# Optimization experiments

Hardware: AMD Instinct MI355X
Metric: run time of the kernel (lower is better)

The kernel has to match this reference:

```python
import jax, jax.numpy as jnp
import numpy as np

EPS = 1e-6
NUM_HEADS = 16

def _phi(x):
    # elu kernel feature map: elu(x) + 1 (ensures positivity)
    return jax.nn.elu(x) + 1.0

def setup_inputs() -> dict:
    key = jax.random.key(0)
    ks = jax.random.split(key, 5)
    B, S, D = 2, 2048, 1024
    scale = 1.0 / np.sqrt(D)  # mimic xavier-ish magnitude
    return {
        "x": jax.random.normal(ks[0], (B, S, D), dtype=jnp.float32),
        "Wq": jax.random.normal(ks[1], (D, D), dtype=jnp.float32) * scale,
        "bq": jnp.zeros((D,), dtype=jnp.float32),
        "Wk": jax.random.normal(ks[2], (D, D), dtype=jnp.float32) * scale,
        "bk": jnp.zeros((D,), dtype=jnp.float32),
        "Wv": jax.random.normal(ks[3], (D, D), dtype=jnp.float32) * scale,
        "bv": jnp.zeros((D,), dtype=jnp.float32),
        "Wo": jax.random.normal(ks[4], (D, D), dtype=jnp.float32) * scale,
        "bo": jnp.zeros((D,), dtype=jnp.float32),
    }

def reference(x, Wq, bq, Wk, bk, Wv, bv, Wo, bo):
    B, S, D = x.shape
    H = NUM_HEADS
    hd = D // H
    # projections (torch Linear: x @ W.T + b)
    q = (x @ Wq.T + bq).reshape(B, S, H, hd).transpose(0, 2, 1, 3)  # [B,H,S,d]
    k = (x @ Wk.T + bk).reshape(B, S, H, hd).transpose(0, 2, 1, 3)
    v = (x @ Wv.T + bv).reshape(B, S, H, hd).transpose(0, 2, 1, 3)
    q = _phi(q)
    k = _phi(k)
    # prefix sums of outer products k_t v_t^T and of k_t (causal linear attention)
    kv_cum = jnp.cumsum(k[..., :, None] * v[..., None, :], axis=2)  # [B,H,S,d,d]
    k_cum = jnp.cumsum(k, axis=2)                                   # [B,H,S,d]
    num = jnp.einsum('bhsd,bhsde->bhse', q, kv_cum)                 # [B,H,S,d]
    den = jnp.einsum('bhsd,bhsd->bhs', q, k_cum)                    # [B,H,S]
    out = num / (den[..., None] + EPS)
    out = out.transpose(0, 2, 1, 3).reshape(B, S, D)
    return out @ Wo.T + bo
```

## Files before the change

### kernel.cpp

```cpp
#include <hip/hip_runtime.h>

typedef unsigned short u16;
typedef __attribute__((ext_vector_type(8))) short bf16x8;
typedef __attribute__((ext_vector_type(4))) float f32x4;

#define DEVI static __device__ __forceinline__

DEVI u16 f2bf(float f) {
  union { float f; unsigned int u; } a; a.f = f;
  unsigned int u = a.u;
  u += 0x7fffu + ((u >> 16) & 1u);
  return (u16)(u >> 16);
}
DEVI float bf2f(u16 h) {
  union { unsigned int u; float f; } a; a.u = ((unsigned int)h) << 16;
  return a.f;
}

DEVI void gload_lds16(const u16* g, u16* l) {
  __builtin_amdgcn_global_load_lds(
      (const __attribute__((address_space(1))) void*)g,
      (__attribute__((address_space(3))) void*)l, 16, 0, 0);
}

DEVI int ldsIdx(int row, int col) {
  return ((col >> 5) << 11) + (row << 5) + (col & 31);
}

struct alignas(8) US4 { u16 a, b, c, d; };

__global__ __launch_bounds__(256) void k_cvt_all(
    const float* __restrict__ x, const float* __restrict__ Wq,
    const float* __restrict__ Wk, const float* __restrict__ Wv,
    const float* __restrict__ Wo, u16* __restrict__ xb, u16* __restrict__ Wqb,
    u16* __restrict__ Wkb, u16* __restrict__ Wvb, u16* __restrict__ Wob) {
  int i = blockIdx.x * 256 + threadIdx.x;
  const float* s;
  u16* d;
  int off;
  if (i < 1048576) {
    s = x; d = xb; off = i;
  } else {
    int j = i - 1048576;
    int w = j >> 18;
    off = j & 262143;
    s = (w == 0) ? Wq : (w == 1) ? Wk : (w == 2) ? Wv : Wo;
    d = (w == 0) ? Wqb : (w == 1) ? Wkb : (w == 2) ? Wvb : Wob;
  }
  f32x4 v = ((const f32x4*)s)[off];
  US4 o{f2bf(v[0]), f2bf(v[1]), f2bf(v[2]), f2bf(v[3])};
  ((US4*)d)[off] = o;
}

__global__ __launch_bounds__(256) void k_gemm_qkv(
    const u16* __restrict__ A, const u16* __restrict__ W,
    const float* __restrict__ bq, const float* __restrict__ bk,
    const float* __restrict__ bv, u16* __restrict__ qb, u16* __restrict__ kb,
    u16* __restrict__ ktb, u16* __restrict__ vtb) {
  __shared__ __align__(16) u16 As[128 * 32];
  __shared__ __align__(16) u16 Bs[128 * 32];
  const int tid = threadIdx.x;
  const int lane = tid & 63;
  const int wave = tid >> 6;
  const int wm = wave >> 1, wn = wave & 1;
  const int m0 = blockIdx.x * 128, n0 = blockIdx.y * 128;
  const int K = 1024;

  f32x4 acc[4][4];
#pragma unroll
  for (int i = 0; i < 4; i++)
#pragma unroll
    for (int j = 0; j < 4; j++) acc[i][j] = (f32x4){0.f, 0.f, 0.f, 0.f};

  const int r0 = tid >> 2, c0 = (tid & 3) * 8;
  const int r1 = (tid + 256) >> 2;
  const u16* Ab0 = A + (size_t)(m0 + r0) * K + c0;
  const u16* Ab1 = A + (size_t)(m0 + r1) * K + c0;
  const u16* Bb0 = W + (size_t)(n0 + r0) * K + c0;
  const u16* Bb1 = W + (size_t)(n0 + r1) * K + c0;
  u16* lA0 = &As[tid * 8];
  u16* lA1 = &As[(tid + 256) * 8];
  u16* lB0 = &Bs[tid * 8];
  u16* lB1 = &Bs[(tid + 256) * 8];

  for (int k0 = 0; k0 < K; k0 += 32) {
    __syncthreads();
    gload_lds16(Ab0 + k0, lA0);
    gload_lds16(Ab1 + k0, lA1);
    gload_lds16(Bb0 + k0, lB0);
    gload_lds16(Bb1 + k0, lB1);
    __syncthreads();
    const int koff = (lane >> 4) * 8;
    bf16x8 af[4], bfr[4];
#pragma unroll
    for (int t = 0; t < 4; t++) {
      af[t] = *(const bf16x8*)&As[(wm * 64 + t * 16 + (lane & 15)) * 32 + koff];
      bfr[t] = *(const bf16x8*)&Bs[(wn * 64 + t * 16 + (lane & 15)) * 32 + koff];
    }
#pragma unroll
    for (int i = 0; i < 4; i++)
#pragma unroll
      for (int j = 0; j < 4; j++)
        acc[i][j] = __builtin_amdgcn_mfma_f32_16x16x32_bf16(af[i], bfr[j],
                                                            acc[i][j], 0, 0, 0);
  }

  const int lr = (lane >> 4) * 4, lc = lane & 15;
  const int region = (int)(blockIdx.y >> 3);
  const float* bias = region == 0 ? bq : (region == 1 ? bk : bv);
#pragma unroll
  for (int j = 0; j < 4; j++) {
    const int colg = n0 + wn * 64 + j * 16 + lc;
    const int cl = colg - (region << 10);
    const float bvv = bias[cl];
#pragma unroll
    for (int i = 0; i < 4; i++) {
      const int row0 = m0 + wm * 64 + i * 16 + lr;
      float v4[4];
#pragma unroll
      for (int r = 0; r < 4; r++) {
        float v = acc[i][j][r] + bvv;
        if (region < 2) v = (v > 0.f) ? (v + 1.f) : __expf(v);
        v4[r] = v;
      }
      if (region == 0) {
#pragma unroll
        for (int r = 0; r < 4; r++)
          qb[(size_t)(row0 + r) * 1024 + cl] = f2bf(v4[r]);
      } else if (region == 1) {
#pragma unroll
        for (int r = 0; r < 4; r++)
          kb[(size_t)(row0 + r) * 1024 + cl] = f2bf(v4[r]);
        US4 o{f2bf(v4[0]), f2bf(v4[1]), f2bf(v4[2]), f2bf(v4[3])};
        *(US4*)&ktb[(size_t)cl * 4096 + row0] = o;
      } else {
        US4 o{f2bf(v4[0]), f2bf(v4[1]), f2bf(v4[2]), f2bf(v4[3])};
        *(US4*)&vtb[(size_t)cl * 4096 + row0] = o;
      }
    }
  }
}

__global__ __launch_bounds__(256) void k_gemm_out(const u16* __restrict__ A,
                                                  const u16* __restrict__ B,
                                                  const float* __restrict__ bias,
                                                  float* __restrict__ C) {
  __shared__ __align__(16) u16 As[64 * 32];
  __shared__ __align__(16) u16 Bs[128 * 32];
  const int tid = threadIdx.x;
  const int lane = tid & 63;
  const int wave = tid >> 6;
  const int wm = wave >> 1, wn = wave & 1;
  const int m0 = blockIdx.x * 64, n0 = blockIdx.y * 128;
  const int K = 1024, N = 1024;
  const int m = lane & 15, quad = lane >> 4;

  f32x4 acc[2][4];
#pragma unroll
  for (int i = 0; i < 2; i++)
#pragma unroll
    for (int j = 0; j < 4; j++) acc[i][j] = (f32x4){0.f, 0.f, 0.f, 0.f};

  const int ra = tid >> 2, c0 = (tid & 3) * 8;
  const int rb1 = (tid + 256) >> 2;
  const u16* Ap = A + (size_t)(m0 + ra) * K + c0;
  const u16* Bp0 = B + (size_t)(n0 + ra) * K + c0;
  const u16* Bp1 = B + (size_t)(n0 + rb1) * K + c0;
  u16* lA = &As[tid * 8];
  u16* lB0 = &Bs[tid * 8];
  u16* lB1 = &Bs[(tid + 256) * 8];

  for (int k0 = 0; k0 < K; k0 += 32) {
    __syncthreads();
    gload_lds16(Ap + k0, lA);
    gload_lds16(Bp0 + k0, lB0);
    gload_lds16(Bp1 + k0, lB1);
    __syncthreads();
    const int koff = quad * 8;
    bf16x8 af[2], bfr[4];
#pragma unroll
    for (int i = 0; i < 2; i++)
      af[i] = *(const bf16x8*)&As[(wm * 32 + i * 16 + m) * 32 + koff];
#pragma unroll
    for (int j = 0; j < 4; j++)
      bfr[j] = *(const bf16x8*)&Bs[(wn * 64 + j * 16 + m) * 32 + koff];
#pragma unroll
    for (int i = 0; i < 2; i++)
#pragma unroll
      for (int j = 0; j < 4; j++)
        acc[i][j] = __builtin_amdgcn_mfma_f32_16x16x32_bf16(af[i], bfr[j],
                                                            acc[i][j], 0, 0, 0);
  }

#pragma unroll
  for (int j = 0; j < 4; j++) {
    const int col = n0 + wn * 64 + j * 16 + m;
    const float bv = bias[col];
#pragma unroll
    for (int i = 0; i < 2; i++) {
      const int row = m0 + wm * 32 + i * 16 + quad * 4;
#pragma unroll
      for (int r = 0; r < 4; r++)
        C[(size_t)(row + r) * N + col] = acc[i][j][r] + bv;
    }
  }
}

__global__ __launch_bounds__(256) void k_chunk2(const u16* __restrict__ ktb,
                                                const u16* __restrict__ vtb,
                                                u16* __restrict__ KVtb,
                                                float* __restrict__ Ks) {
  __shared__ __align__(16) u16 Kt[4096];
  __shared__ __align__(16) u16 Vt[4096];
  __shared__ __align__(16) u16 Ct[64 * 72];
  __shared__ float ksp[64][4];
  const int tid = threadIdx.x, lane = tid & 63, wave = tid >> 6;
  const int ci = blockIdx.x, h = blockIdx.y, b = blockIdx.z;
  const int t0 = b * 2048 + ci * 64, dB = h * 64;
  const int c = (b * 16 + h) * 32 + ci;
  const int row = tid >> 2, colr = (tid & 3) * 8;
#pragma unroll
  for (int r = 0; r < 2; r++) {
    const int col = r * 32 + colr;
    gload_lds16(ktb + (size_t)(dB + row) * 4096 + t0 + col, Kt + r * 2048 + tid * 8);
    gload_lds16(vtb + (size_t)(dB + row) * 4096 + t0 + col, Vt + r * 2048 + tid * 8);
  }
  __syncthreads();
  {
    const int rr = tid >> 2, part = tid & 3;
    float s = 0.f;
#pragma unroll
    for (int t = 0; t < 16; t++) s += bf2f(Kt[ldsIdx(rr, part * 16 + t)]);
    ksp[rr][part] = s;
  }
  __syncthreads();
  if (tid < 64)
    Ks[c * 64 + tid] = ksp[tid][0] + ksp[tid][1] + ksp[tid][2] + ksp[tid][3];

  const int wm = wave >> 1, wn = wave & 1;
  const int md0 = wm * 32, ne0 = wn * 32;
  const int m = lane & 15, quad = lane >> 4;
  f32x4 acc[2][2];
#pragma unroll
  for (int i = 0; i < 2; i++)
#pragma unroll
    for (int j = 0; j < 2; j++) acc[i][j] = (f32x4){0.f, 0.f, 0.f, 0.f};
#pragma unroll
  for (int ks = 0; ks < 2; ks++) {
    const int koff = ks * 32 + quad * 8;
    bf16x8 af[2], bfr[2];
#pragma unroll
    for (int i = 0; i < 2; i++)
      af[i] = *(const bf16x8*)&Kt[ldsIdx(md0 + i * 16 + m, koff)];
#pragma unroll
    for (int j = 0; j < 2; j++)
      bfr[j] = *(const bf16x8*)&Vt[ldsIdx(ne0 + j * 16 + m, koff)];
#pragma unroll
    for (int i = 0; i < 2; i++)
#pragma unroll
      for (int j = 0; j < 2; j++)
        acc[i][j] = __builtin_amdgcn_mfma_f32_16x16x32_bf16(af[i], bfr[j],
                                                            acc[i][j], 0, 0, 0);
  }
#pragma unroll
  for (int i = 0; i < 2; i++)
#pragma unroll
    for (int j = 0; j < 2; j++) {
      const int e = ne0 + j * 16 + m;
      const int d0 = md0 + i * 16 + quad * 4;
      US4 o{f2bf(acc[i][j][0]), f2bf(acc[i][j][1]), f2bf(acc[i][j][2]),
            f2bf(acc[i][j][3])};
      *(US4*)&Ct[e * 72 + d0] = o;
    }
  __syncthreads();
  u16* outp = KVtb + (size_t)c * 4096;
#pragma unroll
  for (int rd = 0; rd < 2; rd++) {
    const int g0 = (tid + rd * 256) * 8;
    const int e = g0 >> 6, d = g0 & 63;
    bf16x8 v = *(const bf16x8*)&Ct[e * 72 + d];
    *(bf16x8*)&outp[g0] = v;
  }
}

__global__ __launch_bounds__(256) void k_prefix(u16* __restrict__ KVtb,
                                                float* __restrict__ Ks) {
  const int slice = blockIdx.x;
  const int bh = blockIdx.y;
  const int tid = threadIdx.x;
  u16* base = KVtb + (size_t)bh * 32 * 4096 + slice * 512 + tid * 2;
  unsigned int vals[32];
#pragma unroll
  for (int ci = 0; ci < 32; ci++)
    vals[ci] = *(const unsigned int*)(base + ci * 4096);
  float r0 = 0.f, r1 = 0.f;
#pragma unroll
  for (int ci = 0; ci < 32; ci++) {
    const float v0 = bf2f((u16)(vals[ci] & 0xffffu));
    const float v1 = bf2f((u16)(vals[ci] >> 16));
    const unsigned int o = (unsigned int)f2bf(r0) | ((unsigned int)f2bf(r1) << 16);
    *(unsigned int*)(base + ci * 4096) = o;
    r0 += v0;
    r1 += v1;
  }
  if (slice == 0 && tid < 64) {
    float* p = Ks + (size_t)bh * 32 * 64 + tid;
    float zb[32];
#pragma unroll
    for (int ci = 0; ci < 32; ci++) zb[ci] = p[ci * 64];
    float zr = 0.f;
#pragma unroll
    for (int ci = 0; ci < 32; ci++) {
      p[ci * 64] = zr;
      zr += zb[ci];
    }
  }
}

__global__ __launch_bounds__(256) void k_attn2(const u16* __restrict__ qb,
                                               const u16* __restrict__ kb,
                                               const u16* __restrict__ vtb,
                                               const u16* __restrict__ KVtb,
                                               const float* __restrict__ Ksg,
                                               u16* __restrict__ Og) {
  __shared__ __align__(16) u16 Qs[4096];
  __shared__ __align__(16) u16 Kr[4096];
  __shared__ __align__(16) u16 Vt[4096];
  __shared__ __align__(16) u16 St[4096];
  __shared__ __align__(16) u16 Am[64 * 72];
  __shared__ float denp[64][4];
  __shared__ float den[64];
  __shared__ float zc[64];
  const int tid = threadIdx.x, lane = tid & 63, wave = tid >> 6;
  const int ci = blockIdx.x, h = blockIdx.y, b = blockIdx.z;
  const int t0 = b * 2048 + ci * 64, colb = h * 64;
  const int c = (b * 16 + h) * 32 + ci;
  const int row = tid >> 2, colr = (tid & 3) * 8;
#pragma unroll
  for (int r = 0; r < 2; r++) {
    const int col = r * 32 + colr;
    gload_lds16(qb + (size_t)(t0 + row) * 1024 + colb + col, Qs + r * 2048 + tid * 8);
    gload_lds16(kb + (size_t)(t0 + row) * 1024 + colb + col, Kr + r * 2048 + tid * 8);
    gload_lds16(vtb + (size_t)(colb + row) * 4096 + t0 + col, Vt + r * 2048 + tid * 8);
    gload_lds16(KVtb + (size_t)c * 4096 + row * 64 + col, St + r * 2048 + tid * 8);
  }
  if (tid < 16) *(f32x4*)&zc[tid * 4] = *(const f32x4*)&Ksg[c * 64 + tid * 4];
  __syncthreads();

  const int wm = wave >> 1, wn = wave & 1;
  const int tm0 = wm * 32, sn0 = wn * 32;
  const int m = lane & 15, quad = lane >> 4;

  f32x4 accA[2][2];
#pragma unroll
  for (int i = 0; i < 2; i++)
#pragma unroll
    for (int j = 0; j < 2; j++) accA[i][j] = (f32x4){0.f, 0.f, 0.f, 0.f};
#pragma unroll
  for (int ks = 0; ks < 2; ks++) {
    const int koff = ks * 32 + quad * 8;
    bf16x8 af[2], bfr[2];
#pragma unroll
    for (int i = 0; i < 2; i++)
      af[i] = *(const bf16x8*)&Qs[ldsIdx(tm0 + i * 16 + m, koff)];
#pragma unroll
    for (int j = 0; j < 2; j++)
      bfr[j] = *(const bf16x8*)&Kr[ldsIdx(sn0 + j * 16 + m, koff)];
#pragma unroll
    for (int i = 0; i < 2; i++)
#pragma unroll
      for (int j = 0; j < 2; j++)
        accA[i][j] = __builtin_amdgcn_mfma_f32_16x16x32_bf16(af[i], bfr[j],
                                                             accA[i][j], 0, 0, 0);
  }
#pragma unroll
  for (int i = 0; i < 2; i++)
#pragma unroll
    for (int j = 0; j < 2; j++) {
      const int s = sn0 + j * 16 + m;
#pragma unroll
      for (int r = 0; r < 4; r++) {
        const int t = tm0 + i * 16 + quad * 4 + r;
        const float v = (s <= t) ? accA[i][j][r] : 0.f;
        Am[t * 72 + s] = f2bf(v);
      }
    }
  __syncthreads();
  {
    const int rr = tid >> 2, part = tid & 3;
    float rs = 0.f, qz = 0.f;
#pragma unroll
    for (int s = 0; s < 16; s++) rs += bf2f(Am[rr * 72 + part * 16 + s]);
#pragma unroll
    for (int d = 0; d < 16; d++)
      qz += bf2f(Qs[ldsIdx(rr, part * 16 + d)]) * zc[part * 16 + d];
    denp[rr][part] = rs + qz;
  }
  __syncthreads();
  if (tid < 64)
    den[tid] =
        denp[tid][0] + denp[tid][1] + denp[tid][2] + denp[tid][3] + 1e-6f;
  __syncthreads();

  f32x4 accO[2][2];
#pragma unroll
  for (int i = 0; i < 2; i++)
#pragma unroll
    for (int j = 0; j < 2; j++) accO[i][j] = (f32x4){0.f, 0.f, 0.f, 0.f};
#pragma unroll
  for (int ks = 0; ks < 2; ks++) {
    const int koff = ks * 32 + quad * 8;
    bf16x8 afA[2], bfV[2], afQ[2], bfS[2];
#pragma unroll
    for (int i = 0; i < 2; i++) {
      afA[i] = *(const bf16x8*)&Am[(tm0 + i * 16 + m) * 72 + koff];
      afQ[i] = *(const bf16x8*)&Qs[ldsIdx(tm0 + i * 16 + m, koff)];
    }
#pragma unroll
    for (int j = 0; j < 2; j++) {
      bfV[j] = *(const bf16x8*)&Vt[ldsIdx(sn0 + j * 16 + m, koff)];
      bfS[j] = *(const bf16x8*)&St[ldsIdx(sn0 + j * 16 + m, koff)];
    }
#pragma unroll
    for (int i = 0; i < 2; i++)
#pragma unroll
      for (int j = 0; j < 2; j++) {
        accO[i][j] = __builtin_amdgcn_mfma_f32_16x16x32_bf16(afA[i], bfV[j],
                                                             accO[i][j], 0, 0, 0);
        accO[i][j] = __builtin_amdgcn_mfma_f32_16x16x32_bf16(afQ[i], bfS[j],
                                                             accO[i][j], 0, 0, 0);
      }
  }
#pragma unroll
  for (int i = 0; i < 2; i++)
#pragma unroll
    for (int r = 0; r < 4; r++) {
      const int t = tm0 + i * 16 + quad * 4 + r;
      const float inv = 1.f / den[t];
#pragma unroll
      for (int j = 0; j < 2; j++) {
        const int e = sn0 + j * 16 + m;
        Og[(size_t)(t0 + t) * 1024 + colb + e] = f2bf(accO[i][j][r] * inv);
      }
    }
}

extern "C" void kernel_launch(void* const* d_in, const int* in_sizes, int n_in,
                              void* d_out, int out_size, void* d_ws,
                              size_t ws_size, hipStream_t stream) {
  const float* x = (const float*)d_in[0];
  const float* Wq = (const float*)d_in[1];
  const float* bq = (const float*)d_in[2];
  const float* Wk = (const float*)d_in[3];
  const float* bk = (const float*)d_in[4];
  const float* Wv = (const float*)d_in[5];
  const float* bv = (const float*)d_in[6];
  const float* Wo = (const float*)d_in[7];
  const float* bo = (const float*)d_in[8];

  char* ws = (char*)d_ws;
  u16* xb = (u16*)(ws + 0);
  u16* ab = xb;
  u16* Wqb = (u16*)(ws + 8388608);
  u16* Wkb = (u16*)(ws + 10485760);
  u16* Wvb = (u16*)(ws + 12582912);
  u16* Wob = (u16*)(ws + 14680064);
  u16* qb = (u16*)(ws + 16777216);
  u16* kb = (u16*)(ws + 25165824);
  u16* ktb = (u16*)(ws + 33554432);
  u16* vtb = (u16*)(ws + 41943040);
  u16* KVtb = (u16*)(ws + 50331648);
  float* Ks = (float*)(ws + 58720256);

  k_cvt_all<<<8192, 256, 0, stream>>>(x, Wq, Wk, Wv, Wo, xb, Wqb, Wkb, Wvb,
                                      Wob);

  k_gemm_qkv<<<dim3(32, 24), 256, 0, stream>>>(xb, Wqb, bq, bk, bv, qb, kb,
                                               ktb, vtb);

  dim3 ga(32, 16, 2);
  k_chunk2<<<ga, 256, 0, stream>>>(ktb, vtb, KVtb, Ks);
  k_prefix<<<dim3(8, 32), 256, 0, stream>>>(KVtb, Ks);
  k_attn2<<<ga, 256, 0, stream>>>(qb, kb, vtb, KVtb, Ks, ab);

  k_gemm_out<<<dim3(64, 8), 256, 0, stream>>>(ab, Wob, bo, (float*)d_out);
}
```

Before: 166.8 us.

## Fuse chunk state, prefix scan and attention into one kernel recomputing prefix state

Replaces the three-kernel chunked linear attention (per-chunk KV outer products, prefix scan over chunks, intra-chunk attention) with one kernel. Each block recomputes the prefix KV state and the key sum by looping over all earlier chunks with double-buffered LDS loads and MFMA; the key sum comes from an MFMA against a ones vector. Blocks are ordered so the longest chunks launch first. This removes two launches and the KVtb/Ks round trips through global memory, but adds quadratic redundant work over chunks (up to 31 iterations per block) and uses more LDS per block.

Result: slower. 171.1 us (+2.6%).

```diff
diff --git a/kernel.cpp b/kernel.cpp
--- a/kernel.cpp
+++ b/kernel.cpp
@@ -206,150 +206,106 @@
   }
 }
 
-__global__ __launch_bounds__(256) void k_chunk2(const u16* __restrict__ ktb,
-                                                const u16* __restrict__ vtb,
-                                                u16* __restrict__ KVtb,
-                                                float* __restrict__ Ks) {
-  __shared__ __align__(16) u16 Kt[4096];
-  __shared__ __align__(16) u16 Vt[4096];
-  __shared__ __align__(16) u16 Ct[64 * 72];
-  __shared__ float ksp[64][4];
-  const int tid = threadIdx.x, lane = tid & 63, wave = tid >> 6;
-  const int ci = blockIdx.x, h = blockIdx.y, b = blockIdx.z;
-  const int t0 = b * 2048 + ci * 64, dB = h * 64;
-  const int c = (b * 16 + h) * 32 + ci;
-  const int row = tid >> 2, colr = (tid & 3) * 8;
-#pragma unroll
-  for (int r = 0; r < 2; r++) {
-    const int col = r * 32 + colr;
-    gload_lds16(ktb + (size_t)(dB + row) * 4096 + t0 + col, Kt + r * 2048 + tid * 8);
-    gload_lds16(vtb + (size_t)(dB + row) * 4096 + t0 + col, Vt + r * 2048 + tid * 8);
-  }
-  __syncthreads();
-  {
-    const int rr = tid >> 2, part = tid & 3;
-    float s = 0.f;
-#pragma unroll
-    for (int t = 0; t < 16; t++) s += bf2f(Kt[ldsIdx(rr, part * 16 + t)]);
-    ksp[rr][part] = s;
-  }
-  __syncthreads();
-  if (tid < 64)
-    Ks[c * 64 + tid] = ksp[tid][0] + ksp[tid][1] + ksp[tid][2] + ksp[tid][3];
-
-  const int wm = wave >> 1, wn = wave & 1;
-  const int md0 = wm * 32, ne0 = wn * 32;
-  const int m = lane & 15, quad = lane >> 4;
-  f32x4 acc[2][2];
-#pragma unroll
-  for (int i = 0; i < 2; i++)
-#pragma unroll
-    for (int j = 0; j < 2; j++) acc[i][j] = (f32x4){0.f, 0.f, 0.f, 0.f};
-#pragma unroll
-  for (int ks = 0; ks < 2; ks++) {
-    const int koff = ks * 32 + quad * 8;
-    bf16x8 af[2], bfr[2];
-#pragma unroll
-    for (int i = 0; i < 2; i++)
-      af[i] = *(const bf16x8*)&Kt[ldsIdx(md0 + i * 16 + m, koff)];
-#pragma unroll
-    for (int j = 0; j < 2; j++)
-      bfr[j] = *(const bf16x8*)&Vt[ldsIdx(ne0 + j * 16 + m, koff)];
-#pragma unroll
-    for (int i = 0; i < 2; i++)
-#pragma unroll
-      for (int j = 0; j < 2; j++)
-        acc[i][j] = __builtin_amdgcn_mfma_f32_16x16x32_bf16(af[i], bfr[j],
-                                                            acc[i][j], 0, 0, 0);
-  }
-#pragma unroll
-  for (int i = 0; i < 2; i++)
-#pragma unroll
-    for (int j = 0; j < 2; j++) {
-      const int e = ne0 + j * 16 + m;
-      const int d0 = md0 + i * 16 + quad * 4;
-      US4 o{f2bf(acc[i][j][0]), f2bf(acc[i][j][1]), f2bf(acc[i][j][2]),
-            f2bf(acc[i][j][3])};
-      *(US4*)&Ct[e * 72 + d0] = o;
-    }
-  __syncthreads();
-  u16* outp = KVtb + (size_t)c * 4096;
-#pragma unroll
-  for (int rd = 0; rd < 2; rd++) {
-    const int g0 = (tid + rd * 256) * 8;
-    const int e = g0 >> 6, d = g0 & 63;
-    bf16x8 v = *(const bf16x8*)&Ct[e * 72 + d];
-    *(bf16x8*)&outp[g0] = v;
-  }
-}
-
-__global__ __launch_bounds__(256) void k_prefix(u16* __restrict__ KVtb,
-                                                float* __restrict__ Ks) {
-  const int slice = blockIdx.x;
-  const int bh = blockIdx.y;
-  const int tid = threadIdx.x;
-  u16* base = KVtb + (size_t)bh * 32 * 4096 + slice * 512 + tid * 2;
-  unsigned int vals[32];
-#pragma unroll
-  for (int ci = 0; ci < 32; ci++)
-    vals[ci] = *(const unsigned int*)(base + ci * 4096);
-  float r0 = 0.f, r1 = 0.f;
-#pragma unroll
-  for (int ci = 0; ci < 32; ci++) {
-    const float v0 = bf2f((u16)(vals[ci] & 0xffffu));
-    const float v1 = bf2f((u16)(vals[ci] >> 16));
-    const unsigned int o = (unsigned int)f2bf(r0) | ((unsigned int)f2bf(r1) << 16);
-    *(unsigned int*)(base + ci * 4096) = o;
-    r0 += v0;
-    r1 += v1;
-  }
-  if (slice == 0 && tid < 64) {
-    float* p = Ks + (size_t)bh * 32 * 64 + tid;
-    float zb[32];
-#pragma unroll
-    for (int ci = 0; ci < 32; ci++) zb[ci] = p[ci * 64];
-    float zr = 0.f;
-#pragma unroll
-    for (int ci = 0; ci < 32; ci++) {
-      p[ci * 64] = zr;
-      zr += zb[ci];
-    }
-  }
-}
-
-__global__ __launch_bounds__(256) void k_attn2(const u16* __restrict__ qb,
-                                               const u16* __restrict__ kb,
-                                               const u16* __restrict__ vtb,
-                                               const u16* __restrict__ KVtb,
-                                               const float* __restrict__ Ksg,
-                                               u16* __restrict__ Og) {
+__global__ __launch_bounds__(256) void k_attn_fused(
+    const u16* __restrict__ qb, const u16* __restrict__ kb,
+    const u16* __restrict__ ktb, const u16* __restrict__ vtb,
+    u16* __restrict__ Og) {
   __shared__ __align__(16) u16 Qs[4096];
   __shared__ __align__(16) u16 Kr[4096];
-  __shared__ __align__(16) u16 Vt[4096];
-  __shared__ __align__(16) u16 St[4096];
-  __shared__ __align__(16) u16 Am[64 * 72];
+  __shared__ __align__(16) u16 Vo[4096];
+  __shared__ __align__(16) u16 KtA[4096];
+  __shared__ __align__(16) u16 VtA[4096];
+  __shared__ __align__(16) u16 pool[9216];
+  __shared__ float zc[64];
   __shared__ float denp[64][4];
   __shared__ float den[64];
-  __shared__ float zc[64];
+  u16* const KtB = pool;
+  u16* const VtB = pool + 4096;
+  u16* const Am = pool;
+  u16* const St = pool + 4608;
+
   const int tid = threadIdx.x, lane = tid & 63, wave = tid >> 6;
-  const int ci = blockIdx.x, h = blockIdx.y, b = blockIdx.z;
+  const int idx = blockIdx.x;
+  const int bh = idx & 31, ci = 31 - (idx >> 5);
+  const int b = bh >> 4, h = bh & 15;
   const int t0 = b * 2048 + ci * 64, colb = h * 64;
-  const int c = (b * 16 + h) * 32 + ci;
   const int row = tid >> 2, colr = (tid & 3) * 8;
+
 #pragma unroll
   for (int r = 0; r < 2; r++) {
     const int col = r * 32 + colr;
     gload_lds16(qb + (size_t)(t0 + row) * 1024 + colb + col, Qs + r * 2048 + tid * 8);
     gload_lds16(kb + (size_t)(t0 + row) * 1024 + colb + col, Kr + r * 2048 + tid * 8);
-    gload_lds16(vtb + (size_t)(colb + row) * 4096 + t0 + col, Vt + r * 2048 + tid * 8);
-    gload_lds16(KVtb + (size_t)c * 4096 + row * 64 + col, St + r * 2048 + tid * 8);
-  }
-  if (tid < 16) *(f32x4*)&zc[tid * 4] = *(const f32x4*)&Ksg[c * 64 + tid * 4];
+    gload_lds16(vtb + (size_t)(colb + row) * 4096 + t0 + col, Vo + r * 2048 + tid * 8);
+  }
+
+  const int wm = wave >> 1, wn = wave & 1;
+  const int m = lane & 15, quad = lane >> 4;
+  const int md0 = wm * 32, ne0 = wn * 32;
+  const int tbase = b * 2048;
+
+  const short ov = (m == 0) ? (short)0x3f80 : (short)0;
+  bf16x8 onesf;
+#pragma unroll
+  for (int t = 0; t < 8; t++) onesf[t] = ov;
+
+  f32x4 accS[2][2];
+#pragma unroll
+  for (int i = 0; i < 2; i++)
+#pragma unroll
+    for (int j = 0; j < 2; j++) accS[i][j] = (f32x4){0.f, 0.f, 0.f, 0.f};
+  f32x4 accZ[2];
+  accZ[0] = (f32x4){0.f, 0.f, 0.f, 0.f};
+  accZ[1] = (f32x4){0.f, 0.f, 0.f, 0.f};
+
+  if (ci > 0) {
+#pragma unroll
+    for (int r = 0; r < 2; r++) {
+      const int col = r * 32 + colr;
+      gload_lds16(ktb + (size_t)(colb + row) * 4096 + tbase + col, KtA + r * 2048 + tid * 8);
+      gload_lds16(vtb + (size_t)(colb + row) * 4096 + tbase + col, VtA + r * 2048 + tid * 8);
+    }
+  }
+  for (int cj = 0; cj < ci; cj++) {
+    __syncthreads();
+    if (cj + 1 < ci) {
+      const int tc = tbase + (cj + 1) * 64;
+      u16* kd = ((cj + 1) & 1) ? KtB : KtA;
+      u16* vd = ((cj + 1) & 1) ? VtB : VtA;
+#pragma unroll
+      for (int r = 0; r < 2; r++) {
+        const int col = r * 32 + colr;
+        gload_lds16(ktb + (size_t)(colb + row) * 4096 + tc + col, kd + r * 2048 + tid * 8);
+        gload_lds16(vtb + (size_t)(colb + row) * 4096 + tc + col, vd + r * 2048 + tid * 8);
+      }
+    }
+    const u16* Ktp = (cj & 1) ? KtB : KtA;
+    const u16* Vtp = (cj & 1) ? VtB : VtA;
+#pragma unroll
+    for (int ks = 0; ks < 2; ks++) {
+      const int koff = ks * 32 + quad * 8;
+      bf16x8 af[2], bfr[2];
+#pragma unroll
+      for (int i = 0; i < 2; i++)
+        af[i] = *(const bf16x8*)&Ktp[ldsIdx(md0 + i * 16 + m, koff)];
+#pragma unroll
+      for (int j = 0; j < 2; j++)
+        bfr[j] = *(const bf16x8*)&Vtp[ldsIdx(ne0 + j * 16 + m, koff)];
+#pragma unroll
+      for (int i = 0; i < 2; i++)
+#pragma unroll
+        for (int j = 0; j < 2; j++)
+          accS[i][j] = __builtin_amdgcn_mfma_f32_16x16x32_bf16(af[i], bfr[j],
+                                                               accS[i][j], 0, 0, 0);
+      if (wn == 0) {
+#pragma unroll
+        for (int i = 0; i < 2; i++)
+          accZ[i] = __builtin_amdgcn_mfma_f32_16x16x32_bf16(af[i], onesf,
+                                                            accZ[i], 0, 0, 0);
+      }
+    }
+  }
   __syncthreads();
-
-  const int wm = wave >> 1, wn = wave & 1;
-  const int tm0 = wm * 32, sn0 = wn * 32;
-  const int m = lane & 15, quad = lane >> 4;
 
   f32x4 accA[2][2];
 #pragma unroll
@@ -362,10 +318,10 @@
     bf16x8 af[2], bfr[2];
 #pragma unroll
     for (int i = 0; i < 2; i++)
-      af[i] = *(const bf16x8*)&Qs[ldsIdx(tm0 + i * 16 + m, koff)];
+      af[i] = *(const bf16x8*)&Qs[ldsIdx(md0 + i * 16 + m, koff)];
 #pragma unroll
     for (int j = 0; j < 2; j++)
-      bfr[j] = *(const bf16x8*)&Kr[ldsIdx(sn0 + j * 16 + m, koff)];
+      bfr[j] = *(const bf16x8*)&Kr[ldsIdx(ne0 + j * 16 + m, koff)];
 #pragma unroll
     for (int i = 0; i < 2; i++)
 #pragma unroll
@@ -377,15 +333,33 @@
   for (int i = 0; i < 2; i++)
 #pragma unroll
     for (int j = 0; j < 2; j++) {
-      const int s = sn0 + j * 16 + m;
+      const int s = ne0 + j * 16 + m;
 #pragma unroll
       for (int r = 0; r < 4; r++) {
-        const int t = tm0 + i * 16 + quad * 4 + r;
+        const int t = md0 + i * 16 + quad * 4 + r;
         const float v = (s <= t) ? accA[i][j][r] : 0.f;
         Am[t * 72 + s] = f2bf(v);
       }
     }
+#pragma unroll
+  for (int i = 0; i < 2; i++)
+#pragma unroll
+    for (int j = 0; j < 2; j++) {
+      const int e = ne0 + j * 16 + m;
+      const int d0 = md0 + i * 16 + quad * 4;
+      US4 o{f2bf(accS[i][j][0]), f2bf(accS[i][j][1]), f2bf(accS[i][j][2]),
+            f2bf(accS[i][j][3])};
+      *(US4*)&St[e * 72 + d0] = o;
+    }
+  if (wn == 0 && m == 0) {
+#pragma unroll
+    for (int i = 0; i < 2; i++)
+#pragma unroll
+      for (int r = 0; r < 4; r++)
+        zc[md0 + i * 16 + quad * 4 + r] = accZ[i][r];
+  }
   __syncthreads();
+
   {
     const int rr = tid >> 2, part = tid & 3;
     float rs = 0.f, qz = 0.f;
@@ -413,13 +387,13 @@
     bf16x8 afA[2], bfV[2], afQ[2], bfS[2];
 #pragma unroll
     for (int i = 0; i < 2; i++) {
-      afA[i] = *(const bf16x8*)&Am[(tm0 + i * 16 + m) * 72 + koff];
-      afQ[i] = *(const bf16x8*)&Qs[ldsIdx(tm0 + i * 16 + m, koff)];
+      afA[i] = *(const bf16x8*)&Am[(md0 + i * 16 + m) * 72 + koff];
+      afQ[i] = *(const bf16x8*)&Qs[ldsIdx(md0 + i * 16 + m, koff)];
     }
 #pragma unroll
     for (int j = 0; j < 2; j++) {
-      bfV[j] = *(const bf16x8*)&Vt[ldsIdx(sn0 + j * 16 + m, koff)];
-      bfS[j] = *(const bf16x8*)&St[ldsIdx(sn0 + j * 16 + m, koff)];
+      bfV[j] = *(const bf16x8*)&Vo[ldsIdx(ne0 + j * 16 + m, koff)];
+      bfS[j] = *(const bf16x8*)&St[(ne0 + j * 16 + m) * 72 + koff];
     }
 #pragma unroll
     for (int i = 0; i < 2; i++)
@@ -435,11 +409,11 @@
   for (int i = 0; i < 2; i++)
 #pragma unroll
     for (int r = 0; r < 4; r++) {
-      const int t = tm0 + i * 16 + quad * 4 + r;
+      const int t = md0 + i * 16 + quad * 4 + r;
       const float inv = 1.f / den[t];
 #pragma unroll
       for (int j = 0; j < 2; j++) {
-        const int e = sn0 + j * 16 + m;
+        const int e = ne0 + j * 16 + m;
         Og[(size_t)(t0 + t) * 1024 + colb + e] = f2bf(accO[i][j][r] * inv);
       }
     }
@@ -469,8 +443,6 @@
   u16* kb = (u16*)(ws + 25165824);
   u16* ktb = (u16*)(ws + 33554432);
   u16* vtb = (u16*)(ws + 41943040);
-  u16* KVtb = (u16*)(ws + 50331648);
-  float* Ks = (float*)(ws + 58720256);
 
   k_cvt_all<<<8192, 256, 0, stream>>>(x, Wq, Wk, Wv, Wo, xb, Wqb, Wkb, Wvb,
                                       Wob);
@@ -478,10 +450,7 @@
   k_gemm_qkv<<<dim3(32, 24), 256, 0, stream>>>(xb, Wqb, bq, bk, bv, qb, kb,
                                                ktb, vtb);
 
-  dim3 ga(32, 16, 2);
-  k_chunk2<<<ga, 256, 0, stream>>>(ktb, vtb, KVtb, Ks);
-  k_prefix<<<dim3(8, 32), 256, 0, stream>>>(KVtb, Ks);
-  k_attn2<<<ga, 256, 0, stream>>>(qb, kb, vtb, KVtb, Ks, ab);
+  k_attn_fused<<<1024, 256, 0, stream>>>(qb, kb, ktb, vtb, ab);
 
   k_gemm_out<<<dim3(64, 8), 256, 0, stream>>>(ab, Wob, bo, (float*)d_out);
 }
```

## Fuse chunk prefix sum into attention kernel by summing prior chunk states

Applied to the files above, without the earlier changes.

Removes the separate k_prefix kernel. Each attention block now sums all preceding chunks' KV states and K sums in fp32 registers, then writes the resulting prefix state into padded LDS. Blocks are launched in reverse chunk order so the blocks with the longest sums start first. This saves one kernel launch and a read-modify-write pass over the chunk states, and accumulates the prefix in fp32 instead of rounding a running sum to bf16. The cost is quadratic redundant reads of chunk states, up to 31 chunks of 8 KB per block.

New measurement: 192.0 us. 15.1% more time.

```diff
diff --git a/kernel.cpp b/kernel.cpp
--- a/kernel.cpp
+++ b/kernel.cpp
@@ -208,7 +208,7 @@
 
 __global__ __launch_bounds__(256) void k_chunk2(const u16* __restrict__ ktb,
                                                 const u16* __restrict__ vtb,
-                                                u16* __restrict__ KVtb,
+                                                u16* __restrict__ KVc,
                                                 float* __restrict__ Ks) {
   __shared__ __align__(16) u16 Kt[4096];
   __shared__ __align__(16) u16 Vt[4096];
@@ -273,7 +273,7 @@
       *(US4*)&Ct[e * 72 + d0] = o;
     }
   __syncthreads();
-  u16* outp = KVtb + (size_t)c * 4096;
+  u16* outp = KVc + (size_t)c * 4096;
 #pragma unroll
   for (int rd = 0; rd < 2; rd++) {
     const int g0 = (tid + rd * 256) * 8;
@@ -283,69 +283,64 @@
   }
 }
 
-__global__ __launch_bounds__(256) void k_prefix(u16* __restrict__ KVtb,
-                                                float* __restrict__ Ks) {
-  const int slice = blockIdx.x;
-  const int bh = blockIdx.y;
-  const int tid = threadIdx.x;
-  u16* base = KVtb + (size_t)bh * 32 * 4096 + slice * 512 + tid * 2;
-  unsigned int vals[32];
-#pragma unroll
-  for (int ci = 0; ci < 32; ci++)
-    vals[ci] = *(const unsigned int*)(base + ci * 4096);
-  float r0 = 0.f, r1 = 0.f;
-#pragma unroll
-  for (int ci = 0; ci < 32; ci++) {
-    const float v0 = bf2f((u16)(vals[ci] & 0xffffu));
-    const float v1 = bf2f((u16)(vals[ci] >> 16));
-    const unsigned int o = (unsigned int)f2bf(r0) | ((unsigned int)f2bf(r1) << 16);
-    *(unsigned int*)(base + ci * 4096) = o;
-    r0 += v0;
-    r1 += v1;
-  }
-  if (slice == 0 && tid < 64) {
-    float* p = Ks + (size_t)bh * 32 * 64 + tid;
-    float zb[32];
-#pragma unroll
-    for (int ci = 0; ci < 32; ci++) zb[ci] = p[ci * 64];
-    float zr = 0.f;
-#pragma unroll
-    for (int ci = 0; ci < 32; ci++) {
-      p[ci * 64] = zr;
-      zr += zb[ci];
-    }
-  }
-}
-
-__global__ __launch_bounds__(256) void k_attn2(const u16* __restrict__ qb,
-                                               const u16* __restrict__ kb,
-                                               const u16* __restrict__ vtb,
-                                               const u16* __restrict__ KVtb,
-                                               const float* __restrict__ Ksg,
-                                               u16* __restrict__ Og) {
+__global__ __launch_bounds__(256) void k_attn3(
+    const u16* __restrict__ qb, const u16* __restrict__ kb,
+    const u16* __restrict__ vtb, const u16* __restrict__ KVc,
+    const float* __restrict__ Ksg, u16* __restrict__ Og) {
   __shared__ __align__(16) u16 Qs[4096];
   __shared__ __align__(16) u16 Kr[4096];
-  __shared__ __align__(16) u16 Vt[4096];
-  __shared__ __align__(16) u16 St[4096];
+  __shared__ __align__(16) u16 Vo[4096];
   __shared__ __align__(16) u16 Am[64 * 72];
+  __shared__ __align__(16) u16 St[64 * 72];
+  __shared__ float zc[64];
   __shared__ float denp[64][4];
   __shared__ float den[64];
-  __shared__ float zc[64];
   const int tid = threadIdx.x, lane = tid & 63, wave = tid >> 6;
-  const int ci = blockIdx.x, h = blockIdx.y, b = blockIdx.z;
+  const int ci = 31 - blockIdx.x, h = blockIdx.y, b = blockIdx.z;
   const int t0 = b * 2048 + ci * 64, colb = h * 64;
-  const int c = (b * 16 + h) * 32 + ci;
+  const int cb = (b * 16 + h) * 32;
   const int row = tid >> 2, colr = (tid & 3) * 8;
+
 #pragma unroll
   for (int r = 0; r < 2; r++) {
     const int col = r * 32 + colr;
     gload_lds16(qb + (size_t)(t0 + row) * 1024 + colb + col, Qs + r * 2048 + tid * 8);
     gload_lds16(kb + (size_t)(t0 + row) * 1024 + colb + col, Kr + r * 2048 + tid * 8);
-    gload_lds16(vtb + (size_t)(colb + row) * 4096 + t0 + col, Vt + r * 2048 + tid * 8);
-    gload_lds16(KVtb + (size_t)c * 4096 + row * 64 + col, St + r * 2048 + tid * 8);
-  }
-  if (tid < 16) *(f32x4*)&zc[tid * 4] = *(const f32x4*)&Ksg[c * 64 + tid * 4];
-  __syncthreads();
+    gload_lds16(vtb + (size_t)(colb + row) * 4096 + t0 + col, Vo + r * 2048 + tid * 8);
+  }
+
+  float S[16];
+#pragma unroll
+  for (int k = 0; k < 16; k++) S[k] = 0.f;
+  {
+    const unsigned int* src =
+        (const unsigned int*)(KVc + (size_t)cb * 4096) + tid;
+    for (int cj = 0; cj < ci; cj++) {
+      const unsigned int* p = src + cj * 2048;
+#pragma unroll
+      for (int k = 0; k < 8; k++) {
+        const unsigned int v = p[k * 256];
+        S[2 * k] += bf2f((u16)(v & 0xffffu));
+        S[2 * k + 1] += bf2f((u16)(v >> 16));
+      }
+    }
+  }
+  if (tid < 64) {
+    float z = 0.f;
+    const float* zp = Ksg + (size_t)cb * 64 + tid;
+    for (int cj = 0; cj < ci; cj++) z += zp[cj * 64];
+    zc[tid] = z;
+  }
+  __syncthreads();
+
+#pragma unroll
+  for (int k = 0; k < 8; k++) {
+    const int u = tid + k * 256;
+    const int e = u >> 5, d = (2 * u) & 63;
+    const unsigned int o =
+        (unsigned int)f2bf(S[2 * k]) | ((unsigned int)f2bf(S[2 * k + 1]) << 16);
+    *(unsigned int*)&St[e * 72 + d] = o;
+  }
 
   const int wm = wave >> 1, wn = wave & 1;
   const int tm0 = wm * 32, sn0 = wn * 32;
@@ -386,6 +381,7 @@
       }
     }
   __syncthreads();
+
   {
     const int rr = tid >> 2, part = tid & 3;
     float rs = 0.f, qz = 0.f;
@@ -418,8 +414,8 @@
     }
 #pragma unroll
     for (int j = 0; j < 2; j++) {
-      bfV[j] = *(const bf16x8*)&Vt[ldsIdx(sn0 + j * 16 + m, koff)];
-      bfS[j] = *(const bf16x8*)&St[ldsIdx(sn0 + j * 16 + m, koff)];
+      bfV[j] = *(const bf16x8*)&Vo[ldsIdx(sn0 + j * 16 + m, koff)];
+      bfS[j] = *(const bf16x8*)&St[(sn0 + j * 16 + m) * 72 + koff];
     }
 #pragma unroll
     for (int i = 0; i < 2; i++)
@@ -469,7 +465,7 @@
   u16* kb = (u16*)(ws + 25165824);
   u16* ktb = (u16*)(ws + 33554432);
   u16* vtb = (u16*)(ws + 41943040);
-  u16* KVtb = (u16*)(ws + 50331648);
+  u16* KVc = (u16*)(ws + 50331648);
   float* Ks = (float*)(ws + 58720256);
 
   k_cvt_all<<<8192, 256, 0, stream>>>(x, Wq, Wk, Wv, Wo, xb, Wqb, Wkb, Wvb,
@@ -479,9 +475,8 @@
                                                ktb, vtb);
 
   dim3 ga(32, 16, 2);
-  k_chunk2<<<ga, 256, 0, stream>>>(ktb, vtb, KVtb, Ks);
-  k_prefix<<<dim3(8, 32), 256, 0, stream>>>(KVtb, Ks);
-  k_attn2<<<ga, 256, 0, stream>>>(qb, kb, vtb, KVtb, Ks, ab);
+  k_chunk2<<<ga, 256, 0, stream>>>(ktb, vtb, KVc, Ks);
+  k_attn3<<<ga, 256, 0, stream>>>(qb, kb, vtb, KVc, Ks, ab);
 
   k_gemm_out<<<dim3(64, 8), 256, 0, stream>>>(ab, Wob, bo, (float*)d_out);
 }
```
